# Kernel tuning notes

Measured on AMD Instinct MI355X. Metric: run time of the kernel, lower is better.

The kernel has to match this reference:

```python
import jax, jax.numpy as jnp
import numpy as np

N_NODES = 50000
N_EDGES = 800000
DIM = 128
N_LAYERS = 5


def setup_inputs() -> dict:
    key = jax.random.key(0)
    k1, k2, k3, k4 = jax.random.split(key, 4)
    x = jax.random.normal(k1, (N_NODES, DIM), dtype=jnp.float32)
    edge_index = jax.random.randint(k2, (2, N_EDGES), 0, N_NODES, dtype=jnp.int64)
    # He-ish scale for stacked GCN layers so activations stay sane
    weights = jax.random.normal(k3, (N_LAYERS, DIM, DIM), dtype=jnp.float32) / jnp.sqrt(jnp.float32(DIM))
    biases = jax.random.normal(k4, (N_LAYERS, DIM), dtype=jnp.float32) * 0.01
    return {"x": x, "edge_index": edge_index, "weights": weights, "biases": biases}


def reference(x, edge_index, weights, biases):
    """5x (GCNConv -> ReLU). GCNConv: out = D^-1/2 (A+I) D^-1/2 (x W) + b."""
    n = x.shape[0]
    src, dst = edge_index[0], edge_index[1]
    # add self-loops (PyG GCNConv default)
    loop = jnp.arange(n, dtype=src.dtype)
    src_f = jnp.concatenate([src, loop])
    dst_f = jnp.concatenate([dst, loop])
    # symmetric normalization based on in-degree (incl. self loops)
    deg = jax.ops.segment_sum(jnp.ones(src_f.shape[0], dtype=x.dtype), dst_f, num_segments=n)
    dinv = jnp.where(deg > 0, jax.lax.rsqrt(deg), 0.0)
    norm = dinv[src_f] * dinv[dst_f]  # [E+N]

    for l in range(weights.shape[0]):
        h = x @ weights[l]                      # [N, D] dense transform
        msg = h[src_f] * norm[:, None]          # gather + scale  [E+N, D]
        x = jax.ops.segment_sum(msg, dst_f, num_segments=n) + biases[l]
        x = jax.nn.relu(x)
    return x
```

## Files before the change

kernel.cpp:

```cpp
#include <hip/hip_runtime.h>
#include <hip/hip_bf16.h>
#include <hip/hip_fp16.h>


#define GCN_DIM 128

typedef short bf16x8 __attribute__((ext_vector_type(8)));
typedef float f32x4 __attribute__((ext_vector_type(4)));

__device__ __forceinline__ unsigned short f2bf(float f) {
    unsigned int u = __float_as_uint(f);
    u += 0x7FFFu + ((u >> 16) & 1u);
    return (unsigned short)(u >> 16);
}
__device__ __forceinline__ float bf2f(unsigned short b) {
    return __uint_as_float(((unsigned int)b) << 16);
}
__device__ __forceinline__ float bflo(unsigned int p) { return __uint_as_float(p << 16); }
__device__ __forceinline__ float bfhi(unsigned int p) { return __uint_as_float(p & 0xFFFF0000u); }

__global__ void count_kernel(const int* __restrict__ dst, int* __restrict__ cnt,
                             int* __restrict__ rank, int E) {
    int e = blockIdx.x * 256 + threadIdx.x;
    if (e < E) rank[e] = atomicAdd(&cnt[dst[e]], 1);
}

__global__ __launch_bounds__(256) void scan_part_kernel(const int* __restrict__ cnt,
                                                        int* __restrict__ loc,
                                                        int* __restrict__ bsum, int n) {
    __shared__ int s[256];
    int t = threadIdx.x;
    int i0 = blockIdx.x * 1024 + t * 4;
    int v0 = (i0 + 0 < n) ? cnt[i0 + 0] : 0;
    int v1 = (i0 + 1 < n) ? cnt[i0 + 1] : 0;
    int v2 = (i0 + 2 < n) ? cnt[i0 + 2] : 0;
    int v3 = (i0 + 3 < n) ? cnt[i0 + 3] : 0;
    int tsum = v0 + v1 + v2 + v3;
    s[t] = tsum;
    __syncthreads();
    for (int d = 1; d < 256; d <<= 1) {
        int u = (t >= d) ? s[t - d] : 0;
        __syncthreads();
        s[t] += u;
        __syncthreads();
    }
    int base = s[t] - tsum;
    if (i0 + 0 < n) loc[i0 + 0] = base; base += v0;
    if (i0 + 1 < n) loc[i0 + 1] = base; base += v1;
    if (i0 + 2 < n) loc[i0 + 2] = base; base += v2;
    if (i0 + 3 < n) loc[i0 + 3] = base;
    if (t == 255) bsum[blockIdx.x] = s[255];
}

__global__ __launch_bounds__(256) void scan_top_kernel(int* __restrict__ bsum, int nb) {
    __shared__ int s[256];
    int t = threadIdx.x;
    int v = (t < nb) ? bsum[t] : 0;
    s[t] = v;
    __syncthreads();
    for (int d = 1; d < 256; d <<= 1) {
        int u = (t >= d) ? s[t - d] : 0;
        __syncthreads();
        s[t] += u;
        __syncthreads();
    }
    if (t < nb) bsum[t] = s[t] - v;
}

__global__ void scan_add_kernel(int* __restrict__ offs,
                                const int* __restrict__ bsum, const int* __restrict__ cnt,
                                float* __restrict__ dinv, int n, int E) {
    int i = blockIdx.x * 256 + threadIdx.x;
    if (i < n) {
        offs[i] = offs[i] + bsum[i >> 10];
        dinv[i] = rsqrtf((float)cnt[i] + 1.0f);
    }
    if (i == 0) offs[n] = E;
}

__global__ void fill_kernel(const int* __restrict__ src, const int* __restrict__ dst,
                            const int* __restrict__ rank, const int* __restrict__ offs,
                            unsigned int* __restrict__ edat, int E) {
    int e = blockIdx.x * 256 + threadIdx.x;
    if (e < E) {
        int d = dst[e];
        int p = offs[d] + rank[e];
        edat[p] = ((unsigned int)src[e]) << 5;
    }
}

__global__ void split_x_kernel(const float* __restrict__ x, unsigned short* __restrict__ xh,
                               unsigned short* __restrict__ xl, int total) {
    int i = (blockIdx.x * 256 + threadIdx.x) * 4;
    if (i >= total) return;
    float4 v = *(const float4*)&x[i];
    ushort4 h4, l4;
    h4.x = f2bf(v.x); l4.x = f2bf(v.x - bf2f(h4.x));
    h4.y = f2bf(v.y); l4.y = f2bf(v.y - bf2f(h4.y));
    h4.z = f2bf(v.z); l4.z = f2bf(v.z - bf2f(h4.z));
    h4.w = f2bf(v.w); l4.w = f2bf(v.w - bf2f(h4.w));
    *(ushort4*)&xh[i] = h4;
    *(ushort4*)&xl[i] = l4;
}

__global__ void wsplit_kernel(const float* __restrict__ Wall, unsigned short* __restrict__ Wfh,
                              unsigned short* __restrict__ Wfl, int total) {
    int idx = blockIdx.x * 256 + threadIdx.x;
    if (idx >= total) return;
    int l = idx >> 14;
    int rem = idx & 16383;
    int k = rem >> 7;
    int nn = rem & 127;
    float v = Wall[idx];
    unsigned short hi = f2bf(v);
    unsigned short lo = f2bf(v - bf2f(hi));
    int t = nn >> 4, ln = nn & 15;
    int ks = k >> 5, q = (k >> 3) & 3, j = k & 7;
    int o = ((((l << 5) | (t << 2) | ks) << 6) | (q << 4) | ln) * 8 + j;
    Wfh[o] = hi;
    Wfl[o] = lo;
}

__global__ __launch_bounds__(256) void gemm_mfma_kernel(
    const unsigned short* __restrict__ xh, const unsigned short* __restrict__ xl,
    const unsigned short* __restrict__ Wfh, const unsigned short* __restrict__ Wfl,
    const float* __restrict__ dinv,
    unsigned short* __restrict__ h, int n) {
    __shared__ unsigned short ldsW[2][8192];
    int tid = threadIdx.x;
    int wave = tid >> 6, lane = tid & 63;
    int q = lane >> 4, ln = lane & 15;
    int rowbase = blockIdx.x * 64 + wave * 16;
    bf16x8 A[4][2];
    {
        int ar = rowbase + ln;
        if (ar >= n) ar = n - 1;
        size_t base = (size_t)ar * GCN_DIM;
#pragma unroll
        for (int ks = 0; ks < 4; ks++) {
            A[ks][0] = *(const bf16x8*)&xh[base + ks * 32 + q * 8];
            A[ks][1] = *(const bf16x8*)&xl[base + ks * 32 + q * 8];
        }
    }
    int node = rowbase + ln;
    float di = (node < n) ? dinv[node] : 0.f;
#pragma unroll
    for (int half = 0; half < 2; half++) {
        if (half) __syncthreads();
        {
            const uint4* gh = (const uint4*)(Wfh + half * 8192);
            const uint4* gl = (const uint4*)(Wfl + half * 8192);
            uint4* sh = (uint4*)ldsW[0];
            uint4* sl = (uint4*)ldsW[1];
#pragma unroll
            for (int r = 0; r < 4; r++) {
                sh[tid + 256 * r] = gh[tid + 256 * r];
                sl[tid + 256 * r] = gl[tid + 256 * r];
            }
        }
        __syncthreads();
#pragma unroll
        for (int tp = 0; tp < 2; tp++) {
            int tta = tp * 2, ttb = tp * 2 + 1;
            f32x4 accA = (f32x4)(0.f), accB = (f32x4)(0.f);
#pragma unroll
            for (int ks = 0; ks < 4; ks++) {
                int foA = ((tta * 4 + ks) * 64 + lane) * 8;
                int foB = ((ttb * 4 + ks) * 64 + lane) * 8;
                bf16x8 bhA = *(const bf16x8*)&ldsW[0][foA];
                bf16x8 blA = *(const bf16x8*)&ldsW[1][foA];
                bf16x8 bhB = *(const bf16x8*)&ldsW[0][foB];
                bf16x8 blB = *(const bf16x8*)&ldsW[1][foB];
                accA = __builtin_amdgcn_mfma_f32_16x16x32_bf16(bhA, A[ks][0], accA, 0, 0, 0);
                accB = __builtin_amdgcn_mfma_f32_16x16x32_bf16(bhB, A[ks][0], accB, 0, 0, 0);
                accA = __builtin_amdgcn_mfma_f32_16x16x32_bf16(bhA, A[ks][1], accA, 0, 0, 0);
                accB = __builtin_amdgcn_mfma_f32_16x16x32_bf16(bhB, A[ks][1], accB, 0, 0, 0);
                accA = __builtin_amdgcn_mfma_f32_16x16x32_bf16(blA, A[ks][0], accA, 0, 0, 0);
                accB = __builtin_amdgcn_mfma_f32_16x16x32_bf16(blB, A[ks][0], accB, 0, 0, 0);
            }
            if (node < n) {
                int ta = half * 4 + tta, tb = half * 4 + ttb;
                ushort4 oA, oB;
                oA.x = f2bf(accA[0] * di); oA.y = f2bf(accA[1] * di);
                oA.z = f2bf(accA[2] * di); oA.w = f2bf(accA[3] * di);
                oB.x = f2bf(accB[0] * di); oB.y = f2bf(accB[1] * di);
                oB.z = f2bf(accB[2] * di); oB.w = f2bf(accB[3] * di);
                *(ushort4*)&h[((size_t)ta * n + node) * 16 + q * 4] = oA;
                *(ushort4*)&h[((size_t)tb * n + node) * 16 + q * 4] = oB;
            }
        }
    }
}

__global__ __launch_bounds__(256) void agg_kernel(
    const unsigned short* __restrict__ h,
    const unsigned int* __restrict__ edat,
    const int* __restrict__ offs,
    const float* __restrict__ dinv, const float* __restrict__ bias,
    unsigned short* __restrict__ xh_out,
    unsigned short* __restrict__ xl_out,
    float* __restrict__ fout, int n) {
    int tid = threadIdx.x;
    int wave = tid >> 6, lane = tid & 63;
    int sub = lane >> 3, ln = lane & 7;
    int slice = blockIdx.x & 7;
    int node = (blockIdx.x >> 3) * 32 + wave * 8 + sub;
    if (node >= n) return;
    const char* hs = (const char*)h + (size_t)slice * n * 32;
    unsigned int fo2 = (unsigned int)(ln << 2);
    float di = dinv[node];
    unsigned int sp = *(const unsigned int*)(hs + (unsigned int)node * 32u + fo2);
    float ax0 = bflo(sp), ay0 = bfhi(sp);
    float ax1 = 0.f, ay1 = 0.f, ax2 = 0.f, ay2 = 0.f, ax3 = 0.f, ay3 = 0.f;
    int s = offs[node], e = offs[node + 1];
    int j = s;
    for (; j + 8 <= e; j += 8) {
        unsigned int v0 = edat[j] + fo2, v1 = edat[j + 1] + fo2;
        unsigned int v2 = edat[j + 2] + fo2, v3 = edat[j + 3] + fo2;
        unsigned int v4 = edat[j + 4] + fo2, v5 = edat[j + 5] + fo2;
        unsigned int v6 = edat[j + 6] + fo2, v7 = edat[j + 7] + fo2;
        unsigned int p0 = *(const unsigned int*)(hs + v0);
        unsigned int p1 = *(const unsigned int*)(hs + v1);
        unsigned int p2 = *(const unsigned int*)(hs + v2);
        unsigned int p3 = *(const unsigned int*)(hs + v3);
        unsigned int p4 = *(const unsigned int*)(hs + v4);
        unsigned int p5 = *(const unsigned int*)(hs + v5);
        unsigned int p6 = *(const unsigned int*)(hs + v6);
        unsigned int p7 = *(const unsigned int*)(hs + v7);
        ax0 += bflo(p0); ay0 += bfhi(p0);
        ax1 += bflo(p1); ay1 += bfhi(p1);
        ax2 += bflo(p2); ay2 += bfhi(p2);
        ax3 += bflo(p3); ay3 += bfhi(p3);
        ax0 += bflo(p4); ay0 += bfhi(p4);
        ax1 += bflo(p5); ay1 += bfhi(p5);
        ax2 += bflo(p6); ay2 += bfhi(p6);
        ax3 += bflo(p7); ay3 += bfhi(p7);
    }
    for (; j + 4 <= e; j += 4) {
        unsigned int v0 = edat[j] + fo2, v1 = edat[j + 1] + fo2;
        unsigned int v2 = edat[j + 2] + fo2, v3 = edat[j + 3] + fo2;
        unsigned int p0 = *(const unsigned int*)(hs + v0);
        unsigned int p1 = *(const unsigned int*)(hs + v1);
        unsigned int p2 = *(const unsigned int*)(hs + v2);
        unsigned int p3 = *(const unsigned int*)(hs + v3);
        ax0 += bflo(p0); ay0 += bfhi(p0);
        ax1 += bflo(p1); ay1 += bfhi(p1);
        ax2 += bflo(p2); ay2 += bfhi(p2);
        ax3 += bflo(p3); ay3 += bfhi(p3);
    }
    for (; j < e; j++) {
        unsigned int v0 = edat[j] + fo2;
        unsigned int p0 = *(const unsigned int*)(hs + v0);
        ax0 += bflo(p0);
        ay0 += bfhi(p0);
    }
    float ax = (ax0 + ax1) + (ax2 + ax3);
    float ay = (ay0 + ay1) + (ay2 + ay3);
    int cg = slice * 16 + (ln << 1);
    float2 b = *(const float2*)&bias[cg];
    float rx = fmaxf(fmaf(di, ax, b.x), 0.f);
    float ry = fmaxf(fmaf(di, ay, b.y), 0.f);
    if (fout) {
        unsigned long long pv = (unsigned long long)__float_as_uint(rx) |
                                ((unsigned long long)__float_as_uint(ry) << 32);
        __builtin_nontemporal_store(pv, (unsigned long long*)&fout[(size_t)node * GCN_DIM + cg]);
    } else {
        unsigned short hx = f2bf(rx), hy = f2bf(ry);
        unsigned int hp = (unsigned int)hx | ((unsigned int)hy << 16);
        unsigned short lx = f2bf(rx - bf2f(hx)), ly = f2bf(ry - bf2f(hy));
        unsigned int lp = (unsigned int)lx | ((unsigned int)ly << 16);
        __builtin_nontemporal_store(hp, (unsigned int*)&xh_out[(size_t)node * GCN_DIM + cg]);
        __builtin_nontemporal_store(lp, (unsigned int*)&xl_out[(size_t)node * GCN_DIM + cg]);
    }
}

extern "C" void kernel_launch(void* const* d_in, const int* in_sizes, int n_in,
                              void* d_out, int out_size, void* d_ws, size_t ws_size,
                              hipStream_t stream) {
    const float* x0    = (const float*)d_in[0];
    const int*   edges = (const int*)d_in[1];
    const float* Wall  = (const float*)d_in[2];
    const float* Ball  = (const float*)d_in[3];
    float* out = (float*)d_out;

    const int n = in_sizes[0] / GCN_DIM;
    const int E = in_sizes[1] / 2;
    const int L = in_sizes[2] / (GCN_DIM * GCN_DIM);

    int*   cnt    = (int*)d_ws;
    float* dinv   = (float*)(cnt + n);
    int*   offs   = (int*)(dinv + n);
    int*   bsum   = offs + n + 16;
    int*   rank   = bsum + 64;
    unsigned int* edat = (unsigned int*)(rank + E);
    unsigned short* h   = (unsigned short*)(edat + E);
    unsigned short* xh  = h  + (size_t)n * GCN_DIM;
    unsigned short* xl  = xh + (size_t)n * GCN_DIM;
    unsigned short* Wfh = xl + (size_t)n * GCN_DIM;
    unsigned short* Wfl = Wfh + (size_t)L * GCN_DIM * GCN_DIM;

    const int* src = edges;
    const int* dst = edges + E;

    int nb_n = (n + 255) / 256;
    int nb_e = (E + 255) / 256;
    int nb_scan = (n + 1023) / 1024;

    hipMemsetAsync(cnt, 0, (size_t)n * sizeof(int), stream);
    count_kernel<<<nb_e, 256, 0, stream>>>(dst, cnt, rank, E);
    scan_part_kernel<<<nb_scan, 256, 0, stream>>>(cnt, offs, bsum, n);
    scan_top_kernel<<<1, 256, 0, stream>>>(bsum, nb_scan);
    scan_add_kernel<<<nb_n, 256, 0, stream>>>(offs, bsum, cnt, dinv, n, E);
    fill_kernel<<<nb_e, 256, 0, stream>>>(src, dst, rank, offs, edat, E);

    int xtotal = n * GCN_DIM;
    split_x_kernel<<<(xtotal / 4 + 255) / 256, 256, 0, stream>>>(x0, xh, xl, xtotal);
    int wtotal = L * GCN_DIM * GCN_DIM;
    wsplit_kernel<<<(wtotal + 255) / 256, 256, 0, stream>>>(Wall, Wfh, Wfl, wtotal);

    int gemm_blocks = (n + 63) / 64;
    int agg_blocks  = ((n + 31) / 32) * 8;

    for (int l = 0; l < L; l++) {
        gemm_mfma_kernel<<<gemm_blocks, 256, 0, stream>>>(
            xh, xl, Wfh + (size_t)l * GCN_DIM * GCN_DIM, Wfl + (size_t)l * GCN_DIM * GCN_DIM,
            dinv, h, n);
        agg_kernel<<<agg_blocks, 256, 0, stream>>>(
            h, edat, offs, dinv, Ball + (size_t)l * GCN_DIM,
            xh, xl, (l == L - 1) ? out : nullptr, n);
    }
}
```

Baseline: 407.7 us.

## Split neighbor gathers across lanes with 16-byte loads and shuffle reduction

The aggregation kernel used to give each lane 4 bytes (two bf16 columns) of a node's 32-byte slice and walk every edge serially. Now pairs of lanes each load 16 bytes of a neighbor row, and four lane groups take different edges in parallel. Partial sums are combined with xor shuffles, and one lane group writes wide 16-byte stores. The aim is fewer, wider gather instructions and a shorter serial loop per node, at the cost of shuffle reductions and idle lanes during the epilogue.

```diff
diff --git a/kernel.cpp b/kernel.cpp
--- a/kernel.cpp
+++ b/kernel.cpp
@@ -7,6 +7,7 @@
 
 typedef short bf16x8 __attribute__((ext_vector_type(8)));
 typedef float f32x4 __attribute__((ext_vector_type(4)));
+typedef unsigned int u32x4 __attribute__((ext_vector_type(4)));
 
 __device__ __forceinline__ unsigned short f2bf(float f) {
     unsigned int u = __float_as_uint(f);
@@ -203,74 +204,92 @@
     int tid = threadIdx.x;
     int wave = tid >> 6, lane = tid & 63;
     int sub = lane >> 3, ln = lane & 7;
+    int p  = ln & 1;
+    int s4 = ln >> 1;
     int slice = blockIdx.x & 7;
     int node = (blockIdx.x >> 3) * 32 + wave * 8 + sub;
     if (node >= n) return;
     const char* hs = (const char*)h + (size_t)slice * n * 32;
-    unsigned int fo2 = (unsigned int)(ln << 2);
+    unsigned int p16 = (unsigned int)(p << 4);
     float di = dinv[node];
-    unsigned int sp = *(const unsigned int*)(hs + (unsigned int)node * 32u + fo2);
-    float ax0 = bflo(sp), ay0 = bfhi(sp);
-    float ax1 = 0.f, ay1 = 0.f, ax2 = 0.f, ay2 = 0.f, ax3 = 0.f, ay3 = 0.f;
+    float a0 = 0.f, a1 = 0.f, a2 = 0.f, a3 = 0.f;
+    float a4 = 0.f, a5 = 0.f, a6 = 0.f, a7 = 0.f;
+#define ACC8(g) do { \
+        a0 += bflo((g).x); a1 += bfhi((g).x); \
+        a2 += bflo((g).y); a3 += bfhi((g).y); \
+        a4 += bflo((g).z); a5 += bfhi((g).z); \
+        a6 += bflo((g).w); a7 += bfhi((g).w); } while (0)
     int s = offs[node], e = offs[node + 1];
     int j = s;
     for (; j + 8 <= e; j += 8) {
-        unsigned int v0 = edat[j] + fo2, v1 = edat[j + 1] + fo2;
-        unsigned int v2 = edat[j + 2] + fo2, v3 = edat[j + 3] + fo2;
-        unsigned int v4 = edat[j + 4] + fo2, v5 = edat[j + 5] + fo2;
-        unsigned int v6 = edat[j + 6] + fo2, v7 = edat[j + 7] + fo2;
-        unsigned int p0 = *(const unsigned int*)(hs + v0);
-        unsigned int p1 = *(const unsigned int*)(hs + v1);
-        unsigned int p2 = *(const unsigned int*)(hs + v2);
-        unsigned int p3 = *(const unsigned int*)(hs + v3);
-        unsigned int p4 = *(const unsigned int*)(hs + v4);
-        unsigned int p5 = *(const unsigned int*)(hs + v5);
-        unsigned int p6 = *(const unsigned int*)(hs + v6);
-        unsigned int p7 = *(const unsigned int*)(hs + v7);
-        ax0 += bflo(p0); ay0 += bfhi(p0);
-        ax1 += bflo(p1); ay1 += bfhi(p1);
-        ax2 += bflo(p2); ay2 += bfhi(p2);
-        ax3 += bflo(p3); ay3 += bfhi(p3);
-        ax0 += bflo(p4); ay0 += bfhi(p4);
-        ax1 += bflo(p5); ay1 += bfhi(p5);
-        ax2 += bflo(p6); ay2 += bfhi(p6);
-        ax3 += bflo(p7); ay3 += bfhi(p7);
-    }
-    for (; j + 4 <= e; j += 4) {
-        unsigned int v0 = edat[j] + fo2, v1 = edat[j + 1] + fo2;
-        unsigned int v2 = edat[j + 2] + fo2, v3 = edat[j + 3] + fo2;
-        unsigned int p0 = *(const unsigned int*)(hs + v0);
-        unsigned int p1 = *(const unsigned int*)(hs + v1);
-        unsigned int p2 = *(const unsigned int*)(hs + v2);
-        unsigned int p3 = *(const unsigned int*)(hs + v3);
-        ax0 += bflo(p0); ay0 += bfhi(p0);
-        ax1 += bflo(p1); ay1 += bfhi(p1);
-        ax2 += bflo(p2); ay2 += bfhi(p2);
-        ax3 += bflo(p3); ay3 += bfhi(p3);
-    }
-    for (; j < e; j++) {
-        unsigned int v0 = edat[j] + fo2;
-        unsigned int p0 = *(const unsigned int*)(hs + v0);
-        ax0 += bflo(p0);
-        ay0 += bfhi(p0);
-    }
-    float ax = (ax0 + ax1) + (ax2 + ax3);
-    float ay = (ay0 + ay1) + (ay2 + ay3);
-    int cg = slice * 16 + (ln << 1);
-    float2 b = *(const float2*)&bias[cg];
-    float rx = fmaxf(fmaf(di, ax, b.x), 0.f);
-    float ry = fmaxf(fmaf(di, ay, b.y), 0.f);
-    if (fout) {
-        unsigned long long pv = (unsigned long long)__float_as_uint(rx) |
-                                ((unsigned long long)__float_as_uint(ry) << 32);
-        __builtin_nontemporal_store(pv, (unsigned long long*)&fout[(size_t)node * GCN_DIM + cg]);
-    } else {
-        unsigned short hx = f2bf(rx), hy = f2bf(ry);
-        unsigned int hp = (unsigned int)hx | ((unsigned int)hy << 16);
-        unsigned short lx = f2bf(rx - bf2f(hx)), ly = f2bf(ry - bf2f(hy));
-        unsigned int lp = (unsigned int)lx | ((unsigned int)ly << 16);
-        __builtin_nontemporal_store(hp, (unsigned int*)&xh_out[(size_t)node * GCN_DIM + cg]);
-        __builtin_nontemporal_store(lp, (unsigned int*)&xl_out[(size_t)node * GCN_DIM + cg]);
+        uint2 od = *(const uint2*)&edat[j + (s4 << 1)];
+        uint4 g0 = *(const uint4*)(hs + (od.x + p16));
+        uint4 g1 = *(const uint4*)(hs + (od.y + p16));
+        __builtin_amdgcn_sched_barrier(0);
+        ACC8(g0);
+        ACC8(g1);
+    }
+    if (j + 4 <= e) {
+        unsigned int od = edat[j + s4];
+        uint4 g0 = *(const uint4*)(hs + (od + p16));
+        ACC8(g0);
+        j += 4;
+    }
+    int rem = e - j;
+    if (s4 < rem) {
+        unsigned int od = edat[j + s4];
+        uint4 g0 = *(const uint4*)(hs + (od + p16));
+        ACC8(g0);
+    }
+    a0 += __shfl_xor(a0, 2); a0 += __shfl_xor(a0, 4);
+    a1 += __shfl_xor(a1, 2); a1 += __shfl_xor(a1, 4);
+    a2 += __shfl_xor(a2, 2); a2 += __shfl_xor(a2, 4);
+    a3 += __shfl_xor(a3, 2); a3 += __shfl_xor(a3, 4);
+    a4 += __shfl_xor(a4, 2); a4 += __shfl_xor(a4, 4);
+    a5 += __shfl_xor(a5, 2); a5 += __shfl_xor(a5, 4);
+    a6 += __shfl_xor(a6, 2); a6 += __shfl_xor(a6, 4);
+    a7 += __shfl_xor(a7, 2); a7 += __shfl_xor(a7, 4);
+    {
+        uint4 sp4 = *(const uint4*)(hs + ((unsigned int)node * 32u + p16));
+        ACC8(sp4);
+    }
+#undef ACC8
+    if (s4 == 0) {
+        int cg = slice * 16 + p * 8;
+        float4 b0 = *(const float4*)&bias[cg];
+        float4 b1 = *(const float4*)&bias[cg + 4];
+        float r0 = fmaxf(fmaf(di, a0, b0.x), 0.f);
+        float r1 = fmaxf(fmaf(di, a1, b0.y), 0.f);
+        float r2 = fmaxf(fmaf(di, a2, b0.z), 0.f);
+        float r3 = fmaxf(fmaf(di, a3, b0.w), 0.f);
+        float r4 = fmaxf(fmaf(di, a4, b1.x), 0.f);
+        float r5 = fmaxf(fmaf(di, a5, b1.y), 0.f);
+        float r6 = fmaxf(fmaf(di, a6, b1.z), 0.f);
+        float r7 = fmaxf(fmaf(di, a7, b1.w), 0.f);
+        if (fout) {
+            f32x4 o0 = {r0, r1, r2, r3};
+            f32x4 o1 = {r4, r5, r6, r7};
+            float* fp = &fout[(size_t)node * GCN_DIM + cg];
+            __builtin_nontemporal_store(o0, (f32x4*)fp);
+            __builtin_nontemporal_store(o1, (f32x4*)(fp + 4));
+        } else {
+            unsigned short h0 = f2bf(r0), h1 = f2bf(r1), h2 = f2bf(r2), h3 = f2bf(r3);
+            unsigned short h4 = f2bf(r4), h5 = f2bf(r5), h6 = f2bf(r6), h7 = f2bf(r7);
+            u32x4 hp = {(unsigned int)h0 | ((unsigned int)h1 << 16),
+                        (unsigned int)h2 | ((unsigned int)h3 << 16),
+                        (unsigned int)h4 | ((unsigned int)h5 << 16),
+                        (unsigned int)h6 | ((unsigned int)h7 << 16)};
+            unsigned short l0 = f2bf(r0 - bf2f(h0)), l1 = f2bf(r1 - bf2f(h1));
+            unsigned short l2 = f2bf(r2 - bf2f(h2)), l3 = f2bf(r3 - bf2f(h3));
+            unsigned short l4 = f2bf(r4 - bf2f(h4)), l5 = f2bf(r5 - bf2f(h5));
+            unsigned short l6 = f2bf(r6 - bf2f(h6)), l7 = f2bf(r7 - bf2f(h7));
+            u32x4 lp = {(unsigned int)l0 | ((unsigned int)l1 << 16),
+                        (unsigned int)l2 | ((unsigned int)l3 << 16),
+                        (unsigned int)l4 | ((unsigned int)l5 << 16),
+                        (unsigned int)l6 | ((unsigned int)l7 << 16)};
+            __builtin_nontemporal_store(hp, (u32x4*)&xh_out[(size_t)node * GCN_DIM + cg]);
+            __builtin_nontemporal_store(lp, (u32x4*)&xl_out[(size_t)node * GCN_DIM + cg]);
+        }
     }
 }
 
```

After: 413.6 us. Within noise of the previous version (+1.5%).
